# Kernel optimization log

Measured on AMD Instinct MI355X. Metric: run time of the kernel, lower is better.

## Reference

```python
import jax, jax.numpy as jnp
import numpy as np

NUM_EMBEDDINGS = 512
EMBEDDING_DIM = 128
COMMITMENT = 0.25
DECAY = 0.99
EPS = 1e-05


def setup_inputs() -> dict:
    key = jax.random.key(0)
    k1, k2 = jax.random.split(key)
    z = jax.random.normal(k1, (32, EMBEDDING_DIM, 64, 64), dtype=jnp.float32)
    embedding = jax.random.normal(k2, (EMBEDDING_DIM, NUM_EMBEDDINGS), dtype=jnp.float32)
    cluster_size = jnp.zeros((NUM_EMBEDDINGS,), dtype=jnp.float32)
    embed_avg = embedding  # buffer initialized as a clone of embedding
    return {"z": z, "embedding": embedding, "cluster_size": cluster_size, "embed_avg": embed_avg}


def reference(z, embedding, cluster_size, embed_avg):
    sg = jax.lax.stop_gradient
    D, K = embedding.shape
    B, C, H, W = z.shape
    z_perm = jnp.transpose(z, (0, 2, 3, 1))          # [B,H,W,D]
    flat_z = z_perm.reshape(-1, D)                    # [N,D]

    distances = ((flat_z ** 2).sum(1, keepdims=True)
                 - 2.0 * (flat_z @ embedding)
                 + (embedding ** 2).sum(0)[None, :])  # [N,K]
    idx = jnp.argmin(distances, axis=1)               # [N]

    # gather codes (equivalent to one-hot @ embedding.T, without materializing one-hot)
    quantized = jnp.take(embedding.T, idx, axis=0).reshape(z_perm.shape)  # [B,H,W,D]
    quantized = jnp.transpose(quantized, (0, 3, 1, 2))                    # [B,D,H,W]

    # EMA codebook update (training branch)
    enc_sum = jax.ops.segment_sum(jnp.ones_like(idx, dtype=flat_z.dtype), idx, num_segments=K)  # [K]
    embed_sum = jax.ops.segment_sum(flat_z, idx, num_segments=K).T                              # [D,K]
    new_cluster_size = cluster_size * DECAY + (1.0 - DECAY) * enc_sum
    new_embed_avg = embed_avg * DECAY + (1.0 - DECAY) * embed_sum
    n = jnp.maximum(new_cluster_size.sum(), 1e-05)
    cs = (new_cluster_size + EPS) / (n + K * EPS) * n
    new_embedding = new_embed_avg / cs[None, :]

    e_latent_loss = jnp.mean((sg(quantized) - z) ** 2)
    q_latent_loss = jnp.mean((quantized - sg(z)) ** 2)
    loss = q_latent_loss + COMMITMENT * e_latent_loss

    quantized_out = z + sg(quantized - z)             # straight-through
    encoding_indices = idx.reshape(B, H, W)
    return (quantized_out, loss, encoding_indices, new_embedding, new_cluster_size, new_embed_avg)
```

## Files before the change

### kernel.cpp

```cpp
#include <hip/hip_runtime.h>
#include <hip/hip_bf16.h>
#include <float.h>

typedef _Float16 f16;
typedef __attribute__((ext_vector_type(8))) _Float16 half8;
typedef __attribute__((ext_vector_type(4))) float floatx4;

#define DIM   128
#define HW    4096
#define NPOS  131072
#define K     512
#define ZSTRIDE_B 524288

#define Q_OFF     0
#define LOSS_OFF  16777216
#define IDX_OFF   16777217
#define NEMB_OFF  16908289
#define NCS_OFF   16973825
#define NEA_OFF   16974337

#define WS_E2    0
#define WS_ENC   512
#define WS_ESUM  1024
#define WS_EHI   1024
#define WS_ELO   33792
#define WS_LOSS  66560
#define WS_NN    66561

#define XST 136

__global__ __launch_bounds__(256) void k_prep(const float* __restrict__ emb,
                                              f16* __restrict__ ehiP,
                                              f16* __restrict__ eloP) {
    int lin = blockIdx.x * 256 + threadIdx.x;
    int d = lin >> 9, k = lin & 511;
    float v = emb[lin];
    f16 h = (f16)v;
    f16 l = (f16)(v - (float)h);
    int g = k >> 4, r = k & 15;
    int dc = d >> 5, w = d & 31, quad = w >> 3, j = w & 7;
    int idx = (g * 4 + dc) * 512 + quad * 128 + r * 8 + j;
    ehiP[idx] = h;
    eloP[idx] = l;
}

__global__ __launch_bounds__(256) void k_e2(const float* __restrict__ emb,
                                            float* __restrict__ e2) {
    __shared__ float part[4][64];
    int kk = blockIdx.x * 64 + (threadIdx.x & 63);
    int dq = threadIdx.x >> 6;
    float s = 0.f;
    #pragma unroll 8
    for (int d = dq * 32; d < dq * 32 + 32; ++d) {
        float v = emb[d * K + kk];
        s = fmaf(v, v, s);
    }
    part[dq][threadIdx.x & 63] = s;
    __syncthreads();
    if (threadIdx.x < 64)
        e2[blockIdx.x * 64 + threadIdx.x] =
            part[0][threadIdx.x] + part[1][threadIdx.x] +
            part[2][threadIdx.x] + part[3][threadIdx.x];
}

__global__ __launch_bounds__(256) void k_assign(const float* __restrict__ z,
                                                const float* __restrict__ emb,
                                                const f16* __restrict__ ehiP,
                                                const f16* __restrict__ eloP,
                                                const float* __restrict__ e2,
                                                float* __restrict__ out,
                                                float* __restrict__ lossAcc) {
    __shared__ f16 xs_h[64 * XST];
    __shared__ f16 xs_l[64 * XST];
    __shared__ float wbD[256];
    __shared__ int   wbI[256];
    __shared__ int   bidx[64];
    __shared__ float wred[4];

    const int tid  = threadIdx.x;
    const int lane = tid & 63;
    const int wv   = tid >> 6;
    const int n0   = blockIdx.x * 64;
    const int b    = n0 >> 12;
    const int hw0  = n0 & 4095;
    const float* zb = z + b * ZSTRIDE_B + hw0;
    const int l15  = lane & 15;
    const int quad = lane >> 4;

    #pragma unroll
    for (int it = 0; it < 16; ++it) {
        int lin = tid + it * 256;
        int i  = lin & 63;
        int dp = lin >> 6;
        float v0 = zb[(2 * dp) * HW + i];
        float v1 = zb[(2 * dp + 1) * HW + i];
        f16 h0 = (f16)v0; f16 l0 = (f16)(v0 - (float)h0);
        f16 h1 = (f16)v1; f16 l1 = (f16)(v1 - (float)h1);
        union { f16 h[2]; unsigned int u; } ph, pl;
        ph.h[0] = h0; ph.h[1] = h1;
        pl.h[0] = l0; pl.h[1] = l1;
        *(unsigned int*)&xs_h[i * XST + 2 * dp] = ph.u;
        *(unsigned int*)&xs_l[i * XST + 2 * dp] = pl.u;
    }
    __syncthreads();

    float bestD[4][4];
    int   bestI[4][4];
    #pragma unroll
    for (int t = 0; t < 4; ++t)
        #pragma unroll
        for (int r = 0; r < 4; ++r) { bestD[t][r] = FLT_MAX; bestI[t][r] = 0x7fffffff; }

    const half8* gh = (const half8*)ehiP;
    const half8* gl = (const half8*)eloP;

    for (int nc = 0; nc < 2; ++nc) {
        floatx4 acc[4][4];
        #pragma unroll
        for (int t = 0; t < 4; ++t)
            #pragma unroll
            for (int nt = 0; nt < 4; ++nt) acc[t][nt] = (floatx4){0.f, 0.f, 0.f, 0.f};

        for (int dc = 0; dc < 4; ++dc) {
            half8 ah[4], al[4];
            #pragma unroll
            for (int t = 0; t < 4; ++t) {
                int off = (t * 16 + l15) * XST + dc * 32 + quad * 8;
                ah[t] = *(const half8*)&xs_h[off];
                al[t] = *(const half8*)&xs_l[off];
            }
            #pragma unroll
            for (int nt = 0; nt < 4; ++nt) {
                int bi = ((nc * 16 + wv * 4 + nt) * 4 + dc) * 64 + lane;
                half8 bh = gh[bi];
                half8 bl = gl[bi];
                #pragma unroll
                for (int t = 0; t < 4; ++t) {
                    acc[t][nt] = __builtin_amdgcn_mfma_f32_16x16x32_f16(ah[t], bh, acc[t][nt], 0, 0, 0);
                    acc[t][nt] = __builtin_amdgcn_mfma_f32_16x16x32_f16(al[t], bh, acc[t][nt], 0, 0, 0);
                    acc[t][nt] = __builtin_amdgcn_mfma_f32_16x16x32_f16(ah[t], bl, acc[t][nt], 0, 0, 0);
                }
            }
        }
        #pragma unroll
        for (int nt = 0; nt < 4; ++nt) {
            int c = nc * 256 + wv * 64 + nt * 16 + l15;
            float ee = e2[c];
            #pragma unroll
            for (int t = 0; t < 4; ++t)
                #pragma unroll
                for (int r = 0; r < 4; ++r) {
                    float s = fmaf(-2.f, acc[t][nt][r], ee);
                    if (s < bestD[t][r]) { bestD[t][r] = s; bestI[t][r] = c; }
                }
        }
    }

    #pragma unroll
    for (int mask = 1; mask <= 8; mask <<= 1) {
        #pragma unroll
        for (int t = 0; t < 4; ++t)
            #pragma unroll
            for (int r = 0; r < 4; ++r) {
                float od = __shfl_xor(bestD[t][r], mask, 64);
                int   oi = __shfl_xor(bestI[t][r], mask, 64);
                if (od < bestD[t][r] || (od == bestD[t][r] && oi < bestI[t][r])) {
                    bestD[t][r] = od; bestI[t][r] = oi;
                }
            }
    }
    if (l15 == 0) {
        #pragma unroll
        for (int t = 0; t < 4; ++t)
            #pragma unroll
            for (int r = 0; r < 4; ++r) {
                int m = t * 16 + quad * 4 + r;
                wbD[wv * 64 + m] = bestD[t][r];
                wbI[wv * 64 + m] = bestI[t][r];
            }
    }
    __syncthreads();
    if (tid < 64) {
        float bd = wbD[tid]; int bi = wbI[tid];
        #pragma unroll
        for (int w = 1; w < 4; ++w) {
            float od = wbD[w * 64 + tid]; int oi = wbI[w * 64 + tid];
            if (od < bd || (od == bd && oi < bi)) { bd = od; bi = oi; }
        }
        bidx[tid] = bi;
        out[IDX_OFF + n0 + tid] = (float)bi;
    }
    __syncthreads();

    float lsum = 0.f;
    #pragma unroll 4
    for (int r = 0; r < 32; ++r) {
        int lin = tid + r * 256;
        int d = lin >> 6, i = lin & 63;
        float q  = emb[d * K + bidx[i]];
        float zz = zb[d * HW + i];
        out[Q_OFF + b * ZSTRIDE_B + d * HW + hw0 + i] = q;
        float df = q - zz;
        lsum = fmaf(df, df, lsum);
    }
    #pragma unroll
    for (int m = 32; m >= 1; m >>= 1) lsum += __shfl_xor(lsum, m, 64);
    if ((tid & 63) == 0) wred[wv] = lsum;
    __syncthreads();
    if (tid == 0) {
        float t = wred[0] + wred[1] + wred[2] + wred[3];
        atomicAdd(lossAcc, t);
    }
}

#define DC 8
__global__ __launch_bounds__(256) void k_ema2(const float* __restrict__ z,
                                              const float* __restrict__ out,
                                              float* __restrict__ enc,
                                              float* __restrict__ esum) {
    __shared__ float acc[DC][K];
    __shared__ float cnt[K];

    const int tid = threadIdx.x;
    const int dchunk = blockIdx.x & 15;
    const int b      = blockIdx.x >> 4;
    const int d0 = dchunk * DC;
    const bool doCnt = (dchunk == 0);

    for (int i = tid; i < DC * K; i += 256) ((float*)acc)[i] = 0.f;
    if (doCnt) for (int i = tid; i < K; i += 256) cnt[i] = 0.f;
    __syncthreads();

    const float* zb  = z + b * ZSTRIDE_B;
    const float* idp = out + IDX_OFF + b * HW;
    for (int t = 0; t < HW; t += 1024) {
        const int p = t + 4 * tid;
        int k0 = (int)idp[p + 0];
        int k1 = (int)idp[p + 1];
        int k2 = (int)idp[p + 2];
        int k3 = (int)idp[p + 3];
        if (doCnt) {
            atomicAdd(&cnt[k0], 1.f); atomicAdd(&cnt[k1], 1.f);
            atomicAdd(&cnt[k2], 1.f); atomicAdd(&cnt[k3], 1.f);
        }
        #pragma unroll
        for (int d = 0; d < DC; ++d) {
            float4 zv = *(const float4*)(zb + (d0 + d) * HW + p);
            atomicAdd(&acc[d][k0], zv.x);
            atomicAdd(&acc[d][k1], zv.y);
            atomicAdd(&acc[d][k2], zv.z);
            atomicAdd(&acc[d][k3], zv.w);
        }
    }
    __syncthreads();

    for (int i = tid; i < DC * K; i += 256) {
        int d = i >> 9, k = i & 511;
        atomicAdd(&esum[(d0 + d) * K + k], acc[d][k]);
    }
    if (doCnt) for (int i = tid; i < K; i += 256) atomicAdd(&enc[i], cnt[i]);
}

__global__ __launch_bounds__(512) void k_final(const float* __restrict__ enc,
                                               const float* __restrict__ cs_in,
                                               const float* __restrict__ lossAcc,
                                               float* __restrict__ out,
                                               float* __restrict__ nnOut) {
    __shared__ float red[512];
    int k = threadIdx.x;
    float ncs = fmaf(cs_in[k], 0.99f, 0.01f * enc[k]);
    red[k] = ncs;
    out[NCS_OFF + k] = ncs;
    __syncthreads();
    for (int s = 256; s > 0; s >>= 1) {
        if (k < s) red[k] += red[k + s];
        __syncthreads();
    }
    if (k == 0) {
        nnOut[0] = fmaxf(red[0], 1e-5f);
        out[LOSS_OFF] = lossAcc[0] * 1.25f / 16777216.0f;
    }
}

__global__ __launch_bounds__(512) void k_final2(const float* __restrict__ esum,
                                                const float* __restrict__ eavg_in,
                                                const float* __restrict__ nnIn,
                                                float* __restrict__ out) {
    int d = blockIdx.x;
    int k = threadIdx.x;
    float nn = nnIn[0];
    float ncs = out[NCS_OFF + k];
    float cs = (ncs + 1e-5f) / (nn + (float)K * 1e-5f) * nn;
    float ea = fmaf(eavg_in[d * K + k], 0.99f, 0.01f * esum[d * K + k]);
    out[NEA_OFF + d * K + k] = ea;
    out[NEMB_OFF + d * K + k] = ea / cs;
}

extern "C" void kernel_launch(void* const* d_in, const int* in_sizes, int n_in,
                              void* d_out, int out_size, void* d_ws, size_t ws_size,
                              hipStream_t stream) {
    const float* z     = (const float*)d_in[0];
    const float* emb   = (const float*)d_in[1];
    const float* cs_in = (const float*)d_in[2];
    const float* eavg  = (const float*)d_in[3];
    float* out = (float*)d_out;
    float* wsF = (float*)d_ws;

    hipMemsetAsync(wsF + WS_ENC, 0, 512 * sizeof(float), stream);
    hipMemsetAsync(wsF + WS_LOSS, 0, sizeof(float), stream);

    k_prep<<<256, 256, 0, stream>>>(emb, (f16*)(wsF + WS_EHI), (f16*)(wsF + WS_ELO));
    k_e2<<<8, 256, 0, stream>>>(emb, wsF + WS_E2);
    k_assign<<<NPOS / 64, 256, 0, stream>>>(z, emb,
                                            (const f16*)(wsF + WS_EHI),
                                            (const f16*)(wsF + WS_ELO),
                                            wsF + WS_E2, out, wsF + WS_LOSS);
    hipMemsetAsync(wsF + WS_ESUM, 0, 65536 * sizeof(float), stream);
    k_ema2<<<512, 256, 0, stream>>>(z, out, wsF + WS_ENC, wsF + WS_ESUM);
    k_final<<<1, 512, 0, stream>>>(wsF + WS_ENC, cs_in, wsF + WS_LOSS,
                                   out, wsF + WS_NN);
    k_final2<<<128, 512, 0, stream>>>(wsF + WS_ESUM, eavg, wsF + WS_NN, out);
}
```

Baseline: 354.2 us.

## Move quantized gather and loss into EMA kernel; fold e2 into prep

The quantized-output gather, its write and the loss reduction move out of the assignment kernel into the EMA scatter kernel. That kernel already streams z per d-chunk, and it now gathers codes from an 8x512 codebook slice staged in shared memory. This avoids reading z a second time and drops the uncoalesced global codebook gathers. Separately, the e2 norm kernel is removed and computed through global atomics inside the prep kernel, with a combined memset that zeroes both e2 and enc. The cost is more shared memory per EMA block, which may lower occupancy, plus atomic contention on e2.

```diff
diff --git a/kernel.cpp b/kernel.cpp
--- a/kernel.cpp
+++ b/kernel.cpp
@@ -31,10 +31,12 @@
 
 __global__ __launch_bounds__(256) void k_prep(const float* __restrict__ emb,
                                               f16* __restrict__ ehiP,
-                                              f16* __restrict__ eloP) {
+                                              f16* __restrict__ eloP,
+                                              float* __restrict__ e2) {
     int lin = blockIdx.x * 256 + threadIdx.x;
     int d = lin >> 9, k = lin & 511;
     float v = emb[lin];
+    atomicAdd(&e2[k], v * v);
     f16 h = (f16)v;
     f16 l = (f16)(v - (float)h);
     int g = k >> 4, r = k & 15;
@@ -44,38 +46,15 @@
     eloP[idx] = l;
 }
 
-__global__ __launch_bounds__(256) void k_e2(const float* __restrict__ emb,
-                                            float* __restrict__ e2) {
-    __shared__ float part[4][64];
-    int kk = blockIdx.x * 64 + (threadIdx.x & 63);
-    int dq = threadIdx.x >> 6;
-    float s = 0.f;
-    #pragma unroll 8
-    for (int d = dq * 32; d < dq * 32 + 32; ++d) {
-        float v = emb[d * K + kk];
-        s = fmaf(v, v, s);
-    }
-    part[dq][threadIdx.x & 63] = s;
-    __syncthreads();
-    if (threadIdx.x < 64)
-        e2[blockIdx.x * 64 + threadIdx.x] =
-            part[0][threadIdx.x] + part[1][threadIdx.x] +
-            part[2][threadIdx.x] + part[3][threadIdx.x];
-}
-
 __global__ __launch_bounds__(256) void k_assign(const float* __restrict__ z,
-                                                const float* __restrict__ emb,
                                                 const f16* __restrict__ ehiP,
                                                 const f16* __restrict__ eloP,
                                                 const float* __restrict__ e2,
-                                                float* __restrict__ out,
-                                                float* __restrict__ lossAcc) {
+                                                float* __restrict__ out) {
     __shared__ f16 xs_h[64 * XST];
     __shared__ f16 xs_l[64 * XST];
     __shared__ float wbD[256];
     __shared__ int   wbI[256];
-    __shared__ int   bidx[64];
-    __shared__ float wred[4];
 
     const int tid  = threadIdx.x;
     const int lane = tid & 63;
@@ -187,52 +166,42 @@
             float od = wbD[w * 64 + tid]; int oi = wbI[w * 64 + tid];
             if (od < bd || (od == bd && oi < bi)) { bd = od; bi = oi; }
         }
-        bidx[tid] = bi;
         out[IDX_OFF + n0 + tid] = (float)bi;
-    }
-    __syncthreads();
-
-    float lsum = 0.f;
-    #pragma unroll 4
-    for (int r = 0; r < 32; ++r) {
-        int lin = tid + r * 256;
-        int d = lin >> 6, i = lin & 63;
-        float q  = emb[d * K + bidx[i]];
-        float zz = zb[d * HW + i];
-        out[Q_OFF + b * ZSTRIDE_B + d * HW + hw0 + i] = q;
-        float df = q - zz;
-        lsum = fmaf(df, df, lsum);
-    }
-    #pragma unroll
-    for (int m = 32; m >= 1; m >>= 1) lsum += __shfl_xor(lsum, m, 64);
-    if ((tid & 63) == 0) wred[wv] = lsum;
-    __syncthreads();
-    if (tid == 0) {
-        float t = wred[0] + wred[1] + wred[2] + wred[3];
-        atomicAdd(lossAcc, t);
     }
 }
 
 #define DC 8
 __global__ __launch_bounds__(256) void k_ema2(const float* __restrict__ z,
-                                              const float* __restrict__ out,
+                                              const float* __restrict__ emb,
+                                              float* __restrict__ out,
                                               float* __restrict__ enc,
-                                              float* __restrict__ esum) {
+                                              float* __restrict__ esum,
+                                              float* __restrict__ lossAcc) {
     __shared__ float acc[DC][K];
+    __shared__ float embs[DC][K];
     __shared__ float cnt[K];
+    __shared__ float wred[4];
 
     const int tid = threadIdx.x;
+    const int lane = tid & 63;
+    const int wv = tid >> 6;
     const int dchunk = blockIdx.x & 15;
     const int b      = blockIdx.x >> 4;
     const int d0 = dchunk * DC;
     const bool doCnt = (dchunk == 0);
 
-    for (int i = tid; i < DC * K; i += 256) ((float*)acc)[i] = 0.f;
+    for (int i = tid; i < DC * K; i += 256) {
+        ((float*)acc)[i] = 0.f;
+        ((float*)embs)[i] = emb[d0 * K + i];
+    }
     if (doCnt) for (int i = tid; i < K; i += 256) cnt[i] = 0.f;
     __syncthreads();
 
     const float* zb  = z + b * ZSTRIDE_B;
     const float* idp = out + IDX_OFF + b * HW;
+    float* qb = out + Q_OFF + b * ZSTRIDE_B;
+    float lsum = 0.f;
+
     for (int t = 0; t < HW; t += 1024) {
         const int p = t + 4 * tid;
         int k0 = (int)idp[p + 0];
@@ -250,9 +219,22 @@
             atomicAdd(&acc[d][k1], zv.y);
             atomicAdd(&acc[d][k2], zv.z);
             atomicAdd(&acc[d][k3], zv.w);
-        }
-    }
-    __syncthreads();
+            float4 qv;
+            qv.x = embs[d][k0]; qv.y = embs[d][k1];
+            qv.z = embs[d][k2]; qv.w = embs[d][k3];
+            *(float4*)(qb + (d0 + d) * HW + p) = qv;
+            float dx = qv.x - zv.x; lsum = fmaf(dx, dx, lsum);
+            float dy = qv.y - zv.y; lsum = fmaf(dy, dy, lsum);
+            float dz2 = qv.z - zv.z; lsum = fmaf(dz2, dz2, lsum);
+            float dw = qv.w - zv.w; lsum = fmaf(dw, dw, lsum);
+        }
+    }
+
+    #pragma unroll
+    for (int m = 32; m >= 1; m >>= 1) lsum += __shfl_xor(lsum, m, 64);
+    if (lane == 0) wred[wv] = lsum;
+    __syncthreads();
+    if (tid == 0) atomicAdd(lossAcc, wred[0] + wred[1] + wred[2] + wred[3]);
 
     for (int i = tid; i < DC * K; i += 256) {
         int d = i >> 9, k = i & 511;
@@ -306,17 +288,18 @@
     float* out = (float*)d_out;
     float* wsF = (float*)d_ws;
 
-    hipMemsetAsync(wsF + WS_ENC, 0, 512 * sizeof(float), stream);
+    hipMemsetAsync(wsF + WS_E2, 0, 1024 * sizeof(float), stream);
     hipMemsetAsync(wsF + WS_LOSS, 0, sizeof(float), stream);
 
-    k_prep<<<256, 256, 0, stream>>>(emb, (f16*)(wsF + WS_EHI), (f16*)(wsF + WS_ELO));
-    k_e2<<<8, 256, 0, stream>>>(emb, wsF + WS_E2);
-    k_assign<<<NPOS / 64, 256, 0, stream>>>(z, emb,
+    k_prep<<<256, 256, 0, stream>>>(emb, (f16*)(wsF + WS_EHI), (f16*)(wsF + WS_ELO),
+                                    wsF + WS_E2);
+    k_assign<<<NPOS / 64, 256, 0, stream>>>(z,
                                             (const f16*)(wsF + WS_EHI),
                                             (const f16*)(wsF + WS_ELO),
-                                            wsF + WS_E2, out, wsF + WS_LOSS);
+                                            wsF + WS_E2, out);
     hipMemsetAsync(wsF + WS_ESUM, 0, 65536 * sizeof(float), stream);
-    k_ema2<<<512, 256, 0, stream>>>(z, out, wsF + WS_ENC, wsF + WS_ESUM);
+    k_ema2<<<512, 256, 0, stream>>>(z, emb, out, wsF + WS_ENC, wsF + WS_ESUM,
+                                    wsF + WS_LOSS);
     k_final<<<1, 512, 0, stream>>>(wsF + WS_ENC, cs_in, wsF + WS_LOSS,
                                    out, wsF + WS_NN);
     k_final2<<<128, 512, 0, stream>>>(wsF + WS_ESUM, eavg, wsF + WS_NN, out);
```

Result: faster. 330.6 us (-6.7%).
